# Kernel tuning notes

Measured on AMD Instinct MI355X. Metric: run time of the kernel, lower is better.

## Reference

```python
import jax, jax.numpy as jnp
import numpy as np

N_NODES = 20000
N_EDGES = 160000
N_GRAPHS = 16
NEG_INF = -1e30


def gcn_conv(x, edge_index, edge_weight, W, b):
    # PyG GCNConv with improved=True: add self-loops with weight 2.0,
    # symmetric degree normalization, linear transform, scatter-add aggregation.
    N = x.shape[0]
    row, col = edge_index[0], edge_index[1]
    loop = jnp.arange(N)
    row = jnp.concatenate([row, loop])
    col = jnp.concatenate([col, loop])
    ew = jnp.concatenate([edge_weight, jnp.full((N,), 2.0, edge_weight.dtype)])
    deg = jax.ops.segment_sum(ew, col, num_segments=N)
    dinv = jnp.where(deg > 0, deg ** -0.5, 0.0)  # deg_inv_sqrt, inf -> 0
    norm = dinv[row] * ew * dinv[col]            # [E+N]
    xl = x @ W                                   # [N, out]
    out = jax.ops.segment_sum(xl[row] * norm[:, None], col, num_segments=N)
    return out + b


def segment_softmax_masked(logits, mask, batch, num_segments):
    # softmax over masked entries, grouped by graph id (torch_geometric softmax
    # after masked_select); unmasked-out positions return 0.
    neg = jnp.asarray(NEG_INF, logits.dtype)
    ml = jnp.where(mask, logits, neg)
    mx = jax.ops.segment_max(ml, batch, num_segments=num_segments)
    ex = jnp.where(mask, jnp.exp(logits - mx[batch]), 0.0)
    s = jax.ops.segment_sum(ex, batch, num_segments=num_segments)
    return ex / jnp.maximum(s[batch], 1e-16)


def setup_inputs() -> dict:
    key = jax.random.key(0)
    ks = jax.random.split(key, 12)
    x = jax.random.normal(ks[0], (N_NODES, 5), dtype=jnp.float32)
    edge_index = jax.random.randint(ks[1], (2, N_EDGES), 0, N_NODES)
    edge_weight = jax.random.uniform(ks[2], (N_EDGES,), dtype=jnp.float32)
    mask = jax.random.randint(ks[3], (N_NODES,), 0, 2).astype(bool)
    batch = jnp.sort(jax.random.randint(ks[4], (N_NODES,), 0, N_GRAPHS))
    # parameters (Glorot-ish scaling)
    W1 = jax.random.normal(ks[5], (5, 1000), dtype=jnp.float32) / np.sqrt(5)
    b1 = jnp.zeros((1000,), jnp.float32)
    W2 = jax.random.normal(ks[6], (1000, 1000), dtype=jnp.float32) / np.sqrt(1000)
    b2 = jnp.zeros((1000,), jnp.float32)
    Wf = jax.random.normal(ks[7], (1000, 1), dtype=jnp.float32) / np.sqrt(1000)
    bf = jnp.zeros((1,), jnp.float32)
    return {"x": x, "edge_weight": edge_weight, "W1": W1, "b1": b1,
            "W2": W2, "b2": b2, "Wf": Wf, "bf": bf,
            "edge_index": edge_index, "mask": mask, "batch": batch}


def reference(x, edge_weight, W1, b1, W2, b2, Wf, bf, edge_index, mask, batch):
    h = jax.nn.relu(gcn_conv(x, edge_index, edge_weight, W1, b1))
    h = jax.nn.relu(gcn_conv(h, edge_index, edge_weight, W2, b2))
    # dropout treated as identity (eval mode) for a deterministic reference
    logits = (h @ Wf + bf)[:, 0]  # [N]
    return segment_softmax_masked(logits, mask, batch, N_GRAPHS)
```

## Files before the change

kernel.cpp:

```cpp
#include <hip/hip_runtime.h>

#define NN 20000
#define NE 160000
#define NG 16
#define KP 1024
#define MT2 160
#define MPAD2 (MT2*128)
#define NBLK 79

typedef __attribute__((ext_vector_type(8))) short bf16x8;
typedef __attribute__((ext_vector_type(4))) float f32x4;

#define GAS __attribute__((address_space(1)))
#define LAS __attribute__((address_space(3)))

__device__ __forceinline__ unsigned short f2bf(float f) {
    unsigned int u = __float_as_uint(f);
    u += 0x7FFFu + ((u >> 16) & 1u);
    return (unsigned short)(u >> 16);
}

__device__ __forceinline__ void gld_lds16(const char* g, char* l) {
    __builtin_amdgcn_global_load_lds((GAS void*)g, (LAS void*)l, 16, 0, 0);
}

__global__ void deg_cnt_kernel(const int* __restrict__ ei, const float* __restrict__ ew,
                               const void* __restrict__ mask, float* deg_r, int* cnt_r,
                               int* flags, int* __restrict__ rank) {
    const int e = blockIdx.x * blockDim.x + threadIdx.x;
    if (e < 5000) {
        const unsigned v = ((const unsigned*)mask)[e];
        if (v > 1u) atomicOr(&flags[0], 1);
        if (v != 0u && v != 0x3F800000u) atomicOr(&flags[1], 1);
    }
    if (e >= NE) return;
    const int rep = blockIdx.x & 3;
    const int c = ei[NE + e];
    atomicAdd(&deg_r[rep * NN + c], ew[e]);
    rank[e] = atomicAdd(&cnt_r[rep * NN + c], 1);
}

__global__ __launch_bounds__(256) void partial_w2t_kernel(const int* __restrict__ cnt_r,
        const float* __restrict__ deg_r, const void* __restrict__ mask,
        const int* __restrict__ flags, int* __restrict__ mtmp,
        float* __restrict__ dinv, int* __restrict__ cnt, int* __restrict__ repoff,
        int* __restrict__ bcnt, int* __restrict__ bmsk,
        const float* __restrict__ W2, unsigned short* __restrict__ W2t,
        float* __restrict__ logitsC) {
    const int bid = blockIdx.x;
    const int t = threadIdx.x;
    if (bid < NBLK) {
        const int i = bid * 256 + t;
        const int f0 = flags[0], f1 = flags[1];
        int c = 0, mv = 0;
        if (i < NN) {
            const int c0 = cnt_r[i],          c1 = cnt_r[NN + i];
            const int c2 = cnt_r[2 * NN + i], c3 = cnt_r[3 * NN + i];
            c = c0 + c1 + c2 + c3;
            cnt[i] = c;
            repoff[i]          = 0;
            repoff[NN + i]     = c0;
            repoff[2 * NN + i] = c0 + c1;
            repoff[3 * NN + i] = c0 + c1 + c2;
            const float d = deg_r[i] + deg_r[NN + i] + deg_r[2 * NN + i] + deg_r[3 * NN + i];
            dinv[i] = 1.0f / sqrtf(2.0f + d);
            if (f0 == 0)      mv = ((const int*)mask)[i] != 0;
            else if (f1 == 0) mv = ((const unsigned*)mask)[i] != 0u;
            else              mv = ((const unsigned char*)mask)[i] != 0;
            mtmp[i] = mv;
        }
        __shared__ int sc[256], sm[256];
        sc[t] = c; sm[t] = mv;
        __syncthreads();
        for (int off = 128; off; off >>= 1) {
            if (t < off) { sc[t] += sc[t + off]; sm[t] += sm[t + off]; }
            __syncthreads();
        }
        if (t == 0) { bcnt[bid] = sc[0]; bmsk[bid] = sm[0]; }
    } else {
        __shared__ float tile[32][33];
        const int bw = bid - NBLK;
        if (t < 20) logitsC[bw * 20 + t] = 0.0f;
        const int n0 = (bw & 31) * 32;
        const int k0 = (bw >> 5) * 32;
        const int tx = t & 31, ty = t >> 5;
#pragma unroll
        for (int j = 0; j < 4; ++j) {
            const int k = k0 + ty + j * 8;
            const int n = n0 + tx;
            tile[ty + j * 8][tx] = (k < 1000 && n < 1000) ? W2[k * 1000 + n] : 0.0f;
        }
        __syncthreads();
#pragma unroll
        for (int j = 0; j < 4; ++j) {
            const int n = n0 + ty + j * 8;
            const int k = k0 + tx;
            W2t[(size_t)n * KP + k] = f2bf(tile[tx][ty + j * 8]);
        }
    }
}

__global__ __launch_bounds__(256) void apply_kernel(const int* __restrict__ cnt,
        const int* __restrict__ mtmp, const int* __restrict__ bcnt,
        const int* __restrict__ bmsk, const int* __restrict__ batch,
        int* __restrict__ offs, int* __restrict__ perm, int* __restrict__ bc,
        int* __restrict__ nm, float* __restrict__ out) {
    const int b = blockIdx.x, t = threadIdx.x;
    __shared__ int pbc[128], pbm[128];
    if (t < 128) {
        pbc[t] = (t < NBLK) ? bcnt[t] : 0;
        pbm[t] = (t < NBLK) ? bmsk[t] : 0;
    }
    __syncthreads();
    for (int off = 1; off < 128; off <<= 1) {
        int uc = 0, um = 0;
        if (t < 128 && t >= off) { uc = pbc[t - off]; um = pbm[t - off]; }
        __syncthreads();
        if (t < 128) { pbc[t] += uc; pbm[t] += um; }
        __syncthreads();
    }
    if (b == 0 && t == 0) nm[0] = pbm[NBLK - 1];
    const int bco = (b == 0) ? 0 : pbc[b - 1];
    const int bmo = (b == 0) ? 0 : pbm[b - 1];
    const int i = b * 256 + t;
    const int c  = (i < NN) ? cnt[i]  : 0;
    const int mv = (i < NN) ? mtmp[i] : 0;
    __shared__ int sc[256], sm[256];
    sc[t] = c; sm[t] = mv;
    __syncthreads();
    for (int off = 1; off < 256; off <<= 1) {
        const int uc = (t >= off) ? sc[t - off] : 0;
        const int um = (t >= off) ? sm[t - off] : 0;
        __syncthreads();
        sc[t] += uc; sm[t] += um;
        __syncthreads();
    }
    if (i < NN) {
        out[i] = 0.0f;
        offs[i] = bco + sc[t] - c;
        if (mv) {
            const int pos = bmo + sm[t] - 1;
            perm[pos] = i;
            bc[pos] = batch[i];
        }
    }
}

__global__ void scatter_kernel(const int* __restrict__ ei, const float* __restrict__ ew,
                               const float* __restrict__ dinv, const int* __restrict__ offs,
                               const int* __restrict__ repoff, const int* __restrict__ rank,
                               int* __restrict__ ssrc, float* __restrict__ snorm) {
    const int e = blockIdx.x * blockDim.x + threadIdx.x;
    if (e >= NE) return;
    const int r = ei[e], c = ei[NE + e];
    const int rep = (e >> 8) & 3;
    const int idx = offs[c] + repoff[rep * NN + c] + rank[e];
    ssrc[idx] = r;
    snorm[idx] = dinv[r] * ew[e] * dinv[c];
}

__global__ __launch_bounds__(256) void axf_kernel(const float* __restrict__ x,
        const int* __restrict__ ssrc, const float* __restrict__ snorm,
        const int* __restrict__ offs, const int* __restrict__ cnt,
        const float* __restrict__ dinv, float* __restrict__ Axf) {
    const int i = blockIdx.x * blockDim.x + threadIdx.x;
    if (i >= NN) return;
    float a0=0,a1=0,a2=0,a3=0,a4=0;
    const int s0 = offs[i], n = cnt[i];
    for (int e = s0; e < s0 + n; ++e) {
        const int r = ssrc[e];
        const float w = snorm[e];
        const float* xr = x + r * 5;
        a0 += w*xr[0]; a1 += w*xr[1]; a2 += w*xr[2]; a3 += w*xr[3]; a4 += w*xr[4];
    }
    const float wl = 2.0f * dinv[i] * dinv[i];
    const float* xi = x + i * 5;
    a0 += wl*xi[0]; a1 += wl*xi[1]; a2 += wl*xi[2]; a3 += wl*xi[3]; a4 += wl*xi[4];
    float* o = Axf + i * 5;
    o[0]=a0; o[1]=a1; o[2]=a2; o[3]=a3; o[4]=a4;
}

__global__ __launch_bounds__(256) void aggW1_kernel(const float* __restrict__ Axf,
        const float* __restrict__ W1, const float* __restrict__ b1,
        const int* __restrict__ ssrc, const float* __restrict__ snorm,
        const int* __restrict__ offs, const int* __restrict__ cnt,
        const float* __restrict__ dinv, const int* __restrict__ perm,
        const int* __restrict__ nm, unsigned short* __restrict__ G) {
    const int tid = threadIdx.x;
    const int wv = tid >> 6;
    const int lane = tid & 63;
    const int half = wv & 1;
    const int jbase = blockIdx.x * 8 + (wv >> 1) * 4;
    const int nmv = nm[0];
    const int npad = (nmv + 127) & ~127;
    if (jbase >= npad) return;

    const int c0 = half * 512 + lane * 8;
    float w1r[5][8], bbr[8];
#pragma unroll
    for (int q = 0; q < 2; ++q) {
        const int c = c0 + q * 4;
        const bool v = (c <= 996);
#pragma unroll
        for (int f = 0; f < 5; ++f) {
            const float4 w4 = v ? *(const float4*)(W1 + f * 1000 + c)
                                : make_float4(0.f, 0.f, 0.f, 0.f);
            w1r[f][q*4+0] = w4.x; w1r[f][q*4+1] = w4.y;
            w1r[f][q*4+2] = w4.z; w1r[f][q*4+3] = w4.w;
        }
        const float4 b4 = v ? *(const float4*)(b1 + c) : make_float4(0.f, 0.f, 0.f, 0.f);
        bbr[q*4+0] = b4.x; bbr[q*4+1] = b4.y; bbr[q*4+2] = b4.z; bbr[q*4+3] = b4.w;
    }

    int iv[4], s0a[4], na[4]; float dva[4];
#pragma unroll
    for (int d = 0; d < 4; ++d) {
        const int j = jbase + d;
        iv[d] = (j < nmv) ? perm[j] : -1;
    }
#pragma unroll
    for (int d = 0; d < 4; ++d) {
        if (iv[d] >= 0) { s0a[d] = offs[iv[d]]; na[d] = cnt[iv[d]]; dva[d] = dinv[iv[d]]; }
        else            { s0a[d] = 0; na[d] = -1; dva[d] = 0.f; }
    }

#pragma unroll
    for (int d = 0; d < 4; ++d) {
        const int j = jbase + d;
        float acc[8];
#pragma unroll
        for (int k = 0; k < 8; ++k) acc[k] = 0.f;
        const int i = iv[d];
        if (i >= 0) {
            const int s0 = s0a[d], n = na[d];
            const int total = n + 1;
            for (int base = 0; base < total; base += 64) {
                const int m = (total - base < 64) ? (total - base) : 64;
                float a0=0.f, a1=0.f, a2=0.f, a3=0.f, a4=0.f, we=0.f;
                if (lane < m) {
                    const int idx = base + lane;
                    int r;
                    if (idx < n) { r = ssrc[s0 + idx]; we = snorm[s0 + idx]; }
                    else         { r = i; we = 2.0f * dva[d] * dva[d]; }
                    const float* axr = Axf + r * 5;
                    a0 = axr[0]; a1 = axr[1]; a2 = axr[2]; a3 = axr[3]; a4 = axr[4];
                }
#pragma unroll 2
                for (int e = 0; e < m; ++e) {
                    const float s0v = __shfl(a0, e);
                    const float s1v = __shfl(a1, e);
                    const float s2v = __shfl(a2, e);
                    const float s3v = __shfl(a3, e);
                    const float s4v = __shfl(a4, e);
                    const float swv = __shfl(we, e);
#pragma unroll
                    for (int k = 0; k < 8; ++k) {
                        const float z = bbr[k] + s0v * w1r[0][k] + s1v * w1r[1][k]
                                      + s2v * w1r[2][k] + s3v * w1r[3][k] + s4v * w1r[4][k];
                        acc[k] += swv * fmaxf(z, 0.f);
                    }
                }
            }
        }
        bf16x8 pk;
#pragma unroll
        for (int k = 0; k < 8; ++k) pk[k] = (short)f2bf(acc[k]);
        *(bf16x8*)(G + (size_t)j * KP + c0) = pk;
    }
}

__global__ __launch_bounds__(256) void gemm_kernel(const unsigned short* __restrict__ A,
                                                   const unsigned short* __restrict__ B,
                                                   const float* __restrict__ b2,
                                                   const float* __restrict__ Wf,
                                                   const int* __restrict__ nm,
                                                   float* __restrict__ logitsC) {
    __shared__ unsigned short As[2048];
    __shared__ unsigned short Bs[4096];
    const int tid = threadIdx.x;
    __shared__ int s_nm;
    if (tid == 0) s_nm = nm[0];
    __syncthreads();
    const int nmv = s_nm;
    const int mstrips = (nmv + 63) >> 6;
    const int bid = blockIdx.x;
    const int tm = (bid >> 6) * 8 + (bid & 7);
    const int tn = (bid >> 3) & 7;
    if (tm >= mstrips) return;
    const int lane = tid & 63;
    const int wv = tid >> 6;
    const int wr = wv >> 1, wc = wv & 1;

    const int chunk = ((tid & 3) ^ ((tid >> 3) & 3)) * 16;
    const int rsub = tid >> 2;
    const char* Ag = (const char*)(A + (size_t)(tm * 64 + rsub) * KP) + chunk;
    const char* Bg = (const char*)(B + (size_t)(tn * 128 + rsub) * KP) + chunk;
    char* AsW = (char*)As + wv * 1024;
    char* BsW = (char*)Bs + wv * 1024;

    f32x4 acc[2][4];
#pragma unroll
    for (int i = 0; i < 2; ++i)
#pragma unroll
        for (int j = 0; j < 4; ++j) acc[i][j] = (f32x4){0.f, 0.f, 0.f, 0.f};

    const int m = lane & 15;
    const int quad = lane >> 4;
    const int sw = quad ^ ((m >> 1) & 3);
    const int aoff = (wr * 32 + m) * 64 + sw * 16;
    const int boff = (wc * 64 + m) * 64 + sw * 16;

    for (int kk = 0; kk < KP; kk += 32) {
        __syncthreads();
        const int kb = kk * 2;
        gld_lds16(Ag + kb,             AsW);
        gld_lds16(Bg + kb,             BsW);
        gld_lds16(Bg + kb + 64 * 2048, BsW + 4096);
        __syncthreads();
        bf16x8 af[2], bfv[4];
#pragma unroll
        for (int mt = 0; mt < 2; ++mt)
            af[mt] = *(const bf16x8*)((const char*)As + aoff + mt * 1024);
#pragma unroll
        for (int nt = 0; nt < 4; ++nt)
            bfv[nt] = *(const bf16x8*)((const char*)Bs + boff + nt * 1024);
#pragma unroll
        for (int mt = 0; mt < 2; ++mt)
#pragma unroll
            for (int nt = 0; nt < 4; ++nt)
                acc[mt][nt] = __builtin_amdgcn_mfma_f32_16x16x32_bf16(af[mt], bfv[nt], acc[mt][nt], 0, 0, 0);
    }

    const int col0 = tn * 128 + wc * 64 + m;
    const int row00 = tm * 64 + wr * 32 + quad * 4;
#pragma unroll
    for (int mt = 0; mt < 2; ++mt) {
        float ps0 = 0.f, ps1 = 0.f, ps2 = 0.f, ps3 = 0.f;
#pragma unroll
        for (int nt = 0; nt < 4; ++nt) {
            const int c = col0 + nt * 16;
            const float bbv = (c < 1000) ? b2[c] : 0.0f;
            const float wfv = (c < 1000) ? Wf[c] : 0.0f;
            ps0 += fmaxf(acc[mt][nt][0] + bbv, 0.f) * wfv;
            ps1 += fmaxf(acc[mt][nt][1] + bbv, 0.f) * wfv;
            ps2 += fmaxf(acc[mt][nt][2] + bbv, 0.f) * wfv;
            ps3 += fmaxf(acc[mt][nt][3] + bbv, 0.f) * wfv;
        }
#pragma unroll
        for (int msk = 1; msk < 16; msk <<= 1) {
            ps0 += __shfl_xor(ps0, msk);
            ps1 += __shfl_xor(ps1, msk);
            ps2 += __shfl_xor(ps2, msk);
            ps3 += __shfl_xor(ps3, msk);
        }
        if (m == 0) {
            const int row = row00 + mt * 16;
            if (row + 0 < nmv) atomicAdd(&logitsC[row + 0], ps0);
            if (row + 1 < nmv) atomicAdd(&logitsC[row + 1], ps1);
            if (row + 2 < nmv) atomicAdd(&logitsC[row + 2], ps2);
            if (row + 3 < nmv) atomicAdd(&logitsC[row + 3], ps3);
        }
    }
}

__global__ __launch_bounds__(256) void softmax_kernel(const float* __restrict__ logitsC,
        const int* __restrict__ perm, const int* __restrict__ bc,
        const int* __restrict__ nm, float* __restrict__ out) {
    const int g = blockIdx.x;
    const int t = threadIdx.x;
    __shared__ int s_lo, s_hi;
    __shared__ float red[4];
    __shared__ float sval;
    if (t == 0) {
        const int nmv = nm[0];
        int lo = 0, hi = nmv;
        while (lo < hi) { const int mid = (lo + hi) >> 1; if (bc[mid] < g) lo = mid + 1; else hi = mid; }
        s_lo = lo;
        int lo2 = lo, hi2 = nmv;
        while (lo2 < hi2) { const int mid = (lo2 + hi2) >> 1; if (bc[mid] < g + 1) lo2 = mid + 1; else hi2 = mid; }
        s_hi = lo2;
    }
    __syncthreads();
    const int lo = s_lo, hi = s_hi;
    float mx = -1e30f;
    for (int i = lo + t; i < hi; i += 256) mx = fmaxf(mx, logitsC[i]);
    for (int off = 32; off; off >>= 1) mx = fmaxf(mx, __shfl_down(mx, off));
    if ((t & 63) == 0) red[t >> 6] = mx;
    __syncthreads();
    if (t == 0) sval = fmaxf(fmaxf(red[0], red[1]), fmaxf(red[2], red[3]));
    __syncthreads();
    mx = sval;
    __syncthreads();
    float sm = 0.f;
    for (int i = lo + t; i < hi; i += 256) sm += expf(logitsC[i] - mx);
    for (int off = 32; off; off >>= 1) sm += __shfl_down(sm, off);
    if ((t & 63) == 0) red[t >> 6] = sm;
    __syncthreads();
    if (t == 0) sval = red[0] + red[1] + red[2] + red[3];
    __syncthreads();
    const float inv = 1.0f / fmaxf(sval, 1e-16f);
    for (int i = lo + t; i < hi; i += 256)
        out[perm[i]] = expf(logitsC[i] - mx) * inv;
}

extern "C" void kernel_launch(void* const* d_in, const int* in_sizes, int n_in,
                              void* d_out, int out_size, void* d_ws, size_t ws_size,
                              hipStream_t stream) {
    (void)in_sizes; (void)n_in; (void)out_size; (void)ws_size;
    const float* x   = (const float*)d_in[0];
    const float* ew  = (const float*)d_in[1];
    const float* W1  = (const float*)d_in[2];
    const float* b1  = (const float*)d_in[3];
    const float* W2  = (const float*)d_in[4];
    const float* b2  = (const float*)d_in[5];
    const float* Wf  = (const float*)d_in[6];
    const int*   ei  = (const int*)d_in[8];
    const void*  mask  = d_in[9];
    const int*   batch = (const int*)d_in[10];
    float* out = (float*)d_out;

    char* p = (char*)d_ws;
    auto carve = [&](size_t bytes) { char* q = p; p += (bytes + 255) & ~(size_t)255; return q; };
    char* zbase = p;
    float* deg_r   = (float*)carve(4 * NN * 4);
    int*   cnt_r   = (int*)carve(4 * NN * 4);
    int*   flags   = (int*)carve(256);
    size_t zspan = (size_t)(p - zbase);
    int*   rank    = (int*)carve(NE * 4);
    int*   repoff  = (int*)carve(4 * NN * 4);
    int*   cnt     = (int*)carve(NN * 4);
    float* logitsC = (float*)carve(MPAD2 * 4);
    int*   offs   = (int*)carve(NN * 4);
    float* dinv   = (float*)carve(NN * 4);
    int*   mtmp   = (int*)carve(NN * 4);
    int*   perm   = (int*)carve(NN * 4);
    int*   bc     = (int*)carve(NN * 4);
    int*   bcnt   = (int*)carve(NBLK * 4);
    int*   bmsk   = (int*)carve(NBLK * 4);
    int*   nmp    = (int*)carve(256);
    int*   ssrc   = (int*)carve(NE * 4);
    float* snorm  = (float*)carve(NE * 4);
    float* Axf    = (float*)carve(NN * 5 * 4);
    unsigned short* W2t = (unsigned short*)carve((size_t)KP * KP * 2);
    unsigned short* G   = (unsigned short*)carve((size_t)MPAD2 * KP * 2);

    hipMemsetAsync(zbase, 0, zspan, stream);
    hipLaunchKernelGGL(deg_cnt_kernel,     dim3(625),       dim3(256), 0, stream, ei, ew, mask, deg_r, cnt_r, flags, rank);
    hipLaunchKernelGGL(partial_w2t_kernel, dim3(NBLK+1024), dim3(256), 0, stream, cnt_r, deg_r, mask, flags, mtmp, dinv, cnt, repoff, bcnt, bmsk, W2, W2t, logitsC);
    hipLaunchKernelGGL(apply_kernel,       dim3(NBLK),      dim3(256), 0, stream, cnt, mtmp, bcnt, bmsk, batch, offs, perm, bc, nmp, out);
    hipLaunchKernelGGL(scatter_kernel,     dim3(625),       dim3(256), 0, stream, ei, ew, dinv, offs, repoff, rank, ssrc, snorm);
    hipLaunchKernelGGL(axf_kernel,         dim3(79),        dim3(256), 0, stream, x, ssrc, snorm, offs, cnt, dinv, Axf);
    hipLaunchKernelGGL(aggW1_kernel,       dim3(MPAD2/8),   dim3(256), 0, stream, Axf, W1, b1, ssrc, snorm, offs, cnt, dinv, perm, nmp, G);
    hipLaunchKernelGGL(gemm_kernel,        dim3(MPAD2/64*8),dim3(256), 0, stream, G, W2t, b2, Wf, nmp, logitsC);
    hipLaunchKernelGGL(softmax_kernel,     dim3(NG),        dim3(256), 0, stream, logitsC, perm, bc, nmp, out);
}
```

Measured before the change: 199.0 us.

## Shrink GEMM M-tile to 32 rows and prefetch first aggregation chunk

The GEMM block tile drops from 64x128 to 32x128, with each wave covering 32 rows by 32 columns. Only two waves load A, and the grid doubles. This raises block count and occupancy for the masked-row GEMM, at the cost of less A/B reuse per block and more B traffic. The aggW1 kernel also hoists the first 64-edge chunk's gathers for all four nodes ahead of the compute loops, overlapping their memory latency.

Result: slower. 222.4 us (+11.7%).

```diff
diff --git a/kernel.cpp b/kernel.cpp
--- a/kernel.cpp
+++ b/kernel.cpp
@@ -224,41 +224,72 @@
         else            { s0a[d] = 0; na[d] = -1; dva[d] = 0.f; }
     }
 
+    float pa0[4], pa1[4], pa2[4], pa3[4], pa4[4], pwe[4];
+    int m0[4];
+#pragma unroll
+    for (int d = 0; d < 4; ++d) {
+        const int n = na[d];
+        const int total = n + 1;
+        const int mm = total < 64 ? total : 64;
+        m0[d] = mm;
+        float a0=0.f, a1=0.f, a2=0.f, a3=0.f, a4=0.f, we=0.f;
+        if (lane < mm) {
+            int r;
+            if (lane < n) { r = ssrc[s0a[d] + lane]; we = snorm[s0a[d] + lane]; }
+            else          { r = iv[d]; we = 2.0f * dva[d] * dva[d]; }
+            const float* axr = Axf + r * 5;
+            a0 = axr[0]; a1 = axr[1]; a2 = axr[2]; a3 = axr[3]; a4 = axr[4];
+        }
+        pa0[d]=a0; pa1[d]=a1; pa2[d]=a2; pa3[d]=a3; pa4[d]=a4; pwe[d]=we;
+    }
+
 #pragma unroll
     for (int d = 0; d < 4; ++d) {
         const int j = jbase + d;
         float acc[8];
 #pragma unroll
         for (int k = 0; k < 8; ++k) acc[k] = 0.f;
-        const int i = iv[d];
-        if (i >= 0) {
-            const int s0 = s0a[d], n = na[d];
-            const int total = n + 1;
-            for (int base = 0; base < total; base += 64) {
-                const int m = (total - base < 64) ? (total - base) : 64;
-                float a0=0.f, a1=0.f, a2=0.f, a3=0.f, a4=0.f, we=0.f;
-                if (lane < m) {
-                    const int idx = base + lane;
-                    int r;
-                    if (idx < n) { r = ssrc[s0 + idx]; we = snorm[s0 + idx]; }
-                    else         { r = i; we = 2.0f * dva[d] * dva[d]; }
-                    const float* axr = Axf + r * 5;
-                    a0 = axr[0]; a1 = axr[1]; a2 = axr[2]; a3 = axr[3]; a4 = axr[4];
-                }
+        const int mfirst = m0[d];
 #pragma unroll 2
-                for (int e = 0; e < m; ++e) {
-                    const float s0v = __shfl(a0, e);
-                    const float s1v = __shfl(a1, e);
-                    const float s2v = __shfl(a2, e);
-                    const float s3v = __shfl(a3, e);
-                    const float s4v = __shfl(a4, e);
-                    const float swv = __shfl(we, e);
-#pragma unroll
-                    for (int k = 0; k < 8; ++k) {
-                        const float z = bbr[k] + s0v * w1r[0][k] + s1v * w1r[1][k]
-                                      + s2v * w1r[2][k] + s3v * w1r[3][k] + s4v * w1r[4][k];
-                        acc[k] += swv * fmaxf(z, 0.f);
-                    }
+        for (int e = 0; e < mfirst; ++e) {
+            const float s0v = __shfl(pa0[d], e);
+            const float s1v = __shfl(pa1[d], e);
+            const float s2v = __shfl(pa2[d], e);
+            const float s3v = __shfl(pa3[d], e);
+            const float s4v = __shfl(pa4[d], e);
+            const float swv = __shfl(pwe[d], e);
+#pragma unroll
+            for (int k = 0; k < 8; ++k) {
+                const float z = bbr[k] + s0v * w1r[0][k] + s1v * w1r[1][k]
+                              + s2v * w1r[2][k] + s3v * w1r[3][k] + s4v * w1r[4][k];
+                acc[k] += swv * fmaxf(z, 0.f);
+            }
+        }
+        const int total = na[d] + 1;
+        for (int base = 64; base < total; base += 64) {
+            const int m = (total - base < 64) ? (total - base) : 64;
+            float a0=0.f, a1=0.f, a2=0.f, a3=0.f, a4=0.f, we=0.f;
+            if (lane < m) {
+                const int idx = base + lane;
+                int r;
+                if (idx < na[d]) { r = ssrc[s0a[d] + idx]; we = snorm[s0a[d] + idx]; }
+                else             { r = iv[d]; we = 2.0f * dva[d] * dva[d]; }
+                const float* axr = Axf + r * 5;
+                a0 = axr[0]; a1 = axr[1]; a2 = axr[2]; a3 = axr[3]; a4 = axr[4];
+            }
+#pragma unroll 2
+            for (int e = 0; e < m; ++e) {
+                const float s0v = __shfl(a0, e);
+                const float s1v = __shfl(a1, e);
+                const float s2v = __shfl(a2, e);
+                const float s3v = __shfl(a3, e);
+                const float s4v = __shfl(a4, e);
+                const float swv = __shfl(we, e);
+#pragma unroll
+                for (int k = 0; k < 8; ++k) {
+                    const float z = bbr[k] + s0v * w1r[0][k] + s1v * w1r[1][k]
+                                  + s2v * w1r[2][k] + s3v * w1r[3][k] + s4v * w1r[4][k];
+                    acc[k] += swv * fmaxf(z, 0.f);
                 }
             }
         }
@@ -275,69 +306,68 @@
                                                    const float* __restrict__ Wf,
                                                    const int* __restrict__ nm,
                                                    float* __restrict__ logitsC) {
-    __shared__ unsigned short As[2048];
+    __shared__ unsigned short As[1024];
     __shared__ unsigned short Bs[4096];
     const int tid = threadIdx.x;
     __shared__ int s_nm;
     if (tid == 0) s_nm = nm[0];
     __syncthreads();
     const int nmv = s_nm;
-    const int mstrips = (nmv + 63) >> 6;
+    const int mstrips = (nmv + 31) >> 5;
     const int bid = blockIdx.x;
     const int tm = (bid >> 6) * 8 + (bid & 7);
     const int tn = (bid >> 3) & 7;
     if (tm >= mstrips) return;
     const int lane = tid & 63;
     const int wv = tid >> 6;
-    const int wr = wv >> 1, wc = wv & 1;
 
     const int chunk = ((tid & 3) ^ ((tid >> 3) & 3)) * 16;
     const int rsub = tid >> 2;
-    const char* Ag = (const char*)(A + (size_t)(tm * 64 + rsub) * KP) + chunk;
+    const char* Ag = (const char*)(A + (size_t)(tm * 32 + (rsub & 31)) * KP) + chunk;
     const char* Bg = (const char*)(B + (size_t)(tn * 128 + rsub) * KP) + chunk;
     char* AsW = (char*)As + wv * 1024;
     char* BsW = (char*)Bs + wv * 1024;
 
-    f32x4 acc[2][4];
+    f32x4 acc[2][2];
 #pragma unroll
     for (int i = 0; i < 2; ++i)
 #pragma unroll
-        for (int j = 0; j < 4; ++j) acc[i][j] = (f32x4){0.f, 0.f, 0.f, 0.f};
+        for (int j = 0; j < 2; ++j) acc[i][j] = (f32x4){0.f, 0.f, 0.f, 0.f};
 
     const int m = lane & 15;
     const int quad = lane >> 4;
     const int sw = quad ^ ((m >> 1) & 3);
-    const int aoff = (wr * 32 + m) * 64 + sw * 16;
-    const int boff = (wc * 64 + m) * 64 + sw * 16;
+    const int aoff = m * 64 + sw * 16;
+    const int boff = (wv * 32 + m) * 64 + sw * 16;
 
     for (int kk = 0; kk < KP; kk += 32) {
         __syncthreads();
         const int kb = kk * 2;
-        gld_lds16(Ag + kb,             AsW);
+        if (wv < 2) gld_lds16(Ag + kb, AsW);
         gld_lds16(Bg + kb,             BsW);
         gld_lds16(Bg + kb + 64 * 2048, BsW + 4096);
         __syncthreads();
-        bf16x8 af[2], bfv[4];
+        bf16x8 af[2], bfv[2];
 #pragma unroll
         for (int mt = 0; mt < 2; ++mt)
             af[mt] = *(const bf16x8*)((const char*)As + aoff + mt * 1024);
 #pragma unroll
-        for (int nt = 0; nt < 4; ++nt)
+        for (int nt = 0; nt < 2; ++nt)
             bfv[nt] = *(const bf16x8*)((const char*)Bs + boff + nt * 1024);
 #pragma unroll
         for (int mt = 0; mt < 2; ++mt)
 #pragma unroll
-            for (int nt = 0; nt < 4; ++nt)
+            for (int nt = 0; nt < 2; ++nt)
                 acc[mt][nt] = __builtin_amdgcn_mfma_f32_16x16x32_bf16(af[mt], bfv[nt], acc[mt][nt], 0, 0, 0);
     }
 
-    const int col0 = tn * 128 + wc * 64 + m;
-    const int row00 = tm * 64 + wr * 32 + quad * 4;
+    const int col0 = tn * 128 + wv * 32 + m;
+    const int row00 = tm * 32 + quad * 4;
 #pragma unroll
     for (int mt = 0; mt < 2; ++mt) {
         float ps0 = 0.f, ps1 = 0.f, ps2 = 0.f, ps3 = 0.f;
 #pragma unroll
-        for (int nt = 0; nt < 4; ++nt) {
+        for (int nt = 0; nt < 2; ++nt) {
             const int c = col0 + nt * 16;
             const float bbv = (c < 1000) ? b2[c] : 0.0f;
             const float wfv = (c < 1000) ? Wf[c] : 0.0f;
@@ -451,6 +481,6 @@
     hipLaunchKernelGGL(scatter_kernel,     dim3(625),       dim3(256), 0, stream, ei, ew, dinv, offs, repoff, rank, ssrc, snorm);
     hipLaunchKernelGGL(axf_kernel,         dim3(79),        dim3(256), 0, stream, x, ssrc, snorm, offs, cnt, dinv, Axf);
     hipLaunchKernelGGL(aggW1_kernel,       dim3(MPAD2/8),   dim3(256), 0, stream, Axf, W1, b1, ssrc, snorm, offs, cnt, dinv, perm, nmp, G);
-    hipLaunchKernelGGL(gemm_kernel,        dim3(MPAD2/64*8),dim3(256), 0, stream, G, W2t, b2, Wf, nmp, logitsC);
+    hipLaunchKernelGGL(gemm_kernel,        dim3(MPAD2/32*8),dim3(256), 0, stream, G, W2t, b2, Wf, nmp, logitsC);
     hipLaunchKernelGGL(softmax_kernel,     dim3(NG),        dim3(256), 0, stream, logitsC, perm, bc, nmp, out);
 }
```

## Precompute first-layer activations to bf16 buffer and gather rows per edge

Applied to the files above, without the earlier changes.

Splits the fused aggregate-and-transform kernel into a per-node kernel that computes relu(Axf·W1+b1) once into a bf16 buffer, and an aggregation kernel that gathers these rows per edge with a software-prefetched next row. This removes the redundant per-edge recomputation of the first-layer activation. In exchange it writes and reads a large intermediate buffer, which adds substantial memory traffic, and it rounds activations to bf16 before aggregation.

Result: slower. 207.8 us (+4.4%).

```diff
diff --git a/kernel.cpp b/kernel.cpp
--- a/kernel.cpp
+++ b/kernel.cpp
@@ -18,6 +18,10 @@
     unsigned int u = __float_as_uint(f);
     u += 0x7FFFu + ((u >> 16) & 1u);
     return (unsigned short)(u >> 16);
+}
+
+__device__ __forceinline__ float bf2f(unsigned short u) {
+    return __uint_as_float(((unsigned)u) << 16);
 }
 
 __device__ __forceinline__ void gld_lds16(const char* g, char* l) {
@@ -180,8 +184,49 @@
     o[0]=a0; o[1]=a1; o[2]=a2; o[3]=a3; o[4]=a4;
 }
 
-__global__ __launch_bounds__(256) void aggW1_kernel(const float* __restrict__ Axf,
+__global__ __launch_bounds__(256) void h1_kernel(const float* __restrict__ Axf,
         const float* __restrict__ W1, const float* __restrict__ b1,
+        unsigned short* __restrict__ H) {
+    const int tid = threadIdx.x;
+    const int wv = tid >> 6;
+    const int lane = tid & 63;
+    const int half = wv & 1;
+    const int ibase = blockIdx.x * 8 + (wv >> 1) * 4;
+    const int c0 = half * 512 + lane * 8;
+    float w1r[5][8], bbr[8];
+#pragma unroll
+    for (int q = 0; q < 2; ++q) {
+        const int c = c0 + q * 4;
+        const bool v = (c <= 996);
+#pragma unroll
+        for (int f = 0; f < 5; ++f) {
+            const float4 w4 = v ? *(const float4*)(W1 + f * 1000 + c)
+                                : make_float4(0.f, 0.f, 0.f, 0.f);
+            w1r[f][q*4+0] = w4.x; w1r[f][q*4+1] = w4.y;
+            w1r[f][q*4+2] = w4.z; w1r[f][q*4+3] = w4.w;
+        }
+        const float4 b4 = v ? *(const float4*)(b1 + c) : make_float4(0.f, 0.f, 0.f, 0.f);
+        bbr[q*4+0] = b4.x; bbr[q*4+1] = b4.y; bbr[q*4+2] = b4.z; bbr[q*4+3] = b4.w;
+    }
+#pragma unroll
+    for (int d = 0; d < 4; ++d) {
+        const int i = ibase + d;
+        if (i < NN) {
+            const float* ax = Axf + (size_t)i * 5;
+            const float a0 = ax[0], a1 = ax[1], a2 = ax[2], a3 = ax[3], a4 = ax[4];
+            bf16x8 pk;
+#pragma unroll
+            for (int k = 0; k < 8; ++k) {
+                const float z = bbr[k] + a0 * w1r[0][k] + a1 * w1r[1][k]
+                              + a2 * w1r[2][k] + a3 * w1r[3][k] + a4 * w1r[4][k];
+                pk[k] = (short)f2bf(fmaxf(z, 0.f));
+            }
+            *(bf16x8*)(H + (size_t)i * KP + c0) = pk;
+        }
+    }
+}
+
+__global__ __launch_bounds__(256) void aggH_kernel(const unsigned short* __restrict__ H,
         const int* __restrict__ ssrc, const float* __restrict__ snorm,
         const int* __restrict__ offs, const int* __restrict__ cnt,
         const float* __restrict__ dinv, const int* __restrict__ perm,
@@ -196,21 +241,7 @@
     if (jbase >= npad) return;
 
     const int c0 = half * 512 + lane * 8;
-    float w1r[5][8], bbr[8];
-#pragma unroll
-    for (int q = 0; q < 2; ++q) {
-        const int c = c0 + q * 4;
-        const bool v = (c <= 996);
-#pragma unroll
-        for (int f = 0; f < 5; ++f) {
-            const float4 w4 = v ? *(const float4*)(W1 + f * 1000 + c)
-                                : make_float4(0.f, 0.f, 0.f, 0.f);
-            w1r[f][q*4+0] = w4.x; w1r[f][q*4+1] = w4.y;
-            w1r[f][q*4+2] = w4.z; w1r[f][q*4+3] = w4.w;
-        }
-        const float4 b4 = v ? *(const float4*)(b1 + c) : make_float4(0.f, 0.f, 0.f, 0.f);
-        bbr[q*4+0] = b4.x; bbr[q*4+1] = b4.y; bbr[q*4+2] = b4.z; bbr[q*4+3] = b4.w;
-    }
+    const unsigned short* Hc = H + c0;
 
     int iv[4], s0a[4], na[4]; float dva[4];
 #pragma unroll
@@ -224,42 +255,63 @@
         else            { s0a[d] = 0; na[d] = -1; dva[d] = 0.f; }
     }
 
+    int pr[4]; float pw[4]; int m0[4];
+#pragma unroll
+    for (int d = 0; d < 4; ++d) {
+        const int n = na[d];
+        const int total = n + 1;
+        const int mm = total < 64 ? total : 64;
+        m0[d] = mm;
+        int r = 0; float w = 0.f;
+        if (lane < mm) {
+            if (lane < n) { r = ssrc[s0a[d] + lane]; w = snorm[s0a[d] + lane]; }
+            else          { r = iv[d]; w = 2.0f * dva[d] * dva[d]; }
+        }
+        pr[d] = r; pw[d] = w;
+    }
+
 #pragma unroll
     for (int d = 0; d < 4; ++d) {
         const int j = jbase + d;
         float acc[8];
 #pragma unroll
         for (int k = 0; k < 8; ++k) acc[k] = 0.f;
-        const int i = iv[d];
-        if (i >= 0) {
-            const int s0 = s0a[d], n = na[d];
-            const int total = n + 1;
-            for (int base = 0; base < total; base += 64) {
-                const int m = (total - base < 64) ? (total - base) : 64;
-                float a0=0.f, a1=0.f, a2=0.f, a3=0.f, a4=0.f, we=0.f;
-                if (lane < m) {
-                    const int idx = base + lane;
-                    int r;
-                    if (idx < n) { r = ssrc[s0 + idx]; we = snorm[s0 + idx]; }
-                    else         { r = i; we = 2.0f * dva[d] * dva[d]; }
-                    const float* axr = Axf + r * 5;
-                    a0 = axr[0]; a1 = axr[1]; a2 = axr[2]; a3 = axr[3]; a4 = axr[4];
-                }
-#pragma unroll 2
-                for (int e = 0; e < m; ++e) {
-                    const float s0v = __shfl(a0, e);
-                    const float s1v = __shfl(a1, e);
-                    const float s2v = __shfl(a2, e);
-                    const float s3v = __shfl(a3, e);
-                    const float s4v = __shfl(a4, e);
-                    const float swv = __shfl(we, e);
-#pragma unroll
-                    for (int k = 0; k < 8; ++k) {
-                        const float z = bbr[k] + s0v * w1r[0][k] + s1v * w1r[1][k]
-                                      + s2v * w1r[2][k] + s3v * w1r[3][k] + s4v * w1r[4][k];
-                        acc[k] += swv * fmaxf(z, 0.f);
-                    }
-                }
+        const int mfirst = m0[d];
+        bf16x8 hcur = {};
+        float wcur = 0.f;
+        if (mfirst > 0) {
+            const int r0 = __shfl(pr[d], 0);
+            wcur = __shfl(pw[d], 0);
+            hcur = *(const bf16x8*)(Hc + (size_t)r0 * KP);
+        }
+        for (int e = 0; e < mfirst; ++e) {
+            bf16x8 hn = hcur; float wn = 0.f;
+            if (e + 1 < mfirst) {
+                const int rn = __shfl(pr[d], e + 1);
+                wn = __shfl(pw[d], e + 1);
+                hn = *(const bf16x8*)(Hc + (size_t)rn * KP);
+            }
+#pragma unroll
+            for (int k = 0; k < 8; ++k)
+                acc[k] += wcur * bf2f((unsigned short)hcur[k]);
+            hcur = hn; wcur = wn;
+        }
+        const int total = na[d] + 1;
+        for (int base = 64; base < total; base += 64) {
+            const int m = (total - base < 64) ? (total - base) : 64;
+            int r = 0; float w = 0.f;
+            if (lane < m) {
+                const int idx = base + lane;
+                if (idx < na[d]) { r = ssrc[s0a[d] + idx]; w = snorm[s0a[d] + idx]; }
+                else             { r = iv[d]; w = 2.0f * dva[d] * dva[d]; }
+            }
+            for (int e = 0; e < m; ++e) {
+                const int rv = __shfl(r, e);
+                const float wvv = __shfl(w, e);
+                const bf16x8 h = *(const bf16x8*)(Hc + (size_t)rv * KP);
+#pragma unroll
+                for (int k = 0; k < 8; ++k)
+                    acc[k] += wvv * bf2f((unsigned short)h[k]);
             }
         }
         bf16x8 pk;
@@ -442,6 +494,7 @@
     float* snorm  = (float*)carve(NE * 4);
     float* Axf    = (float*)carve(NN * 5 * 4);
     unsigned short* W2t = (unsigned short*)carve((size_t)KP * KP * 2);
+    unsigned short* H   = (unsigned short*)carve((size_t)NN * KP * 2);
     unsigned short* G   = (unsigned short*)carve((size_t)MPAD2 * KP * 2);
 
     hipMemsetAsync(zbase, 0, zspan, stream);
@@ -450,7 +503,8 @@
     hipLaunchKernelGGL(apply_kernel,       dim3(NBLK),      dim3(256), 0, stream, cnt, mtmp, bcnt, bmsk, batch, offs, perm, bc, nmp, out);
     hipLaunchKernelGGL(scatter_kernel,     dim3(625),       dim3(256), 0, stream, ei, ew, dinv, offs, repoff, rank, ssrc, snorm);
     hipLaunchKernelGGL(axf_kernel,         dim3(79),        dim3(256), 0, stream, x, ssrc, snorm, offs, cnt, dinv, Axf);
-    hipLaunchKernelGGL(aggW1_kernel,       dim3(MPAD2/8),   dim3(256), 0, stream, Axf, W1, b1, ssrc, snorm, offs, cnt, dinv, perm, nmp, G);
+    hipLaunchKernelGGL(h1_kernel,          dim3(NN/8),      dim3(256), 0, stream, Axf, W1, b1, H);
+    hipLaunchKernelGGL(aggH_kernel,        dim3(MPAD2/8),   dim3(256), 0, stream, H, ssrc, snorm, offs, cnt, dinv, perm, nmp, G);
     hipLaunchKernelGGL(gemm_kernel,        dim3(MPAD2/64*8),dim3(256), 0, stream, G, W2t, b2, Wf, nmp, logitsC);
     hipLaunchKernelGGL(softmax_kernel,     dim3(NG),        dim3(256), 0, stream, logitsC, perm, bc, nmp, out);
 }
```
